# Kernel tuning notes

Measured on AMD Instinct MI355X. Metric: run time of the kernel, lower is better.

The kernel has to match this reference:

```python
import jax, jax.numpy as jnp
import numpy as np

B, S, M, H, P, T = 32, 400, 400, 200, 16, 4

def setup_inputs() -> dict:
    key = jax.random.key(0)
    ks = jax.random.split(key, 20)
    sc = 0.05
    inp = {
        'att': jax.random.normal(ks[0], (B, S, M), jnp.float32),
        'mod': jax.random.normal(ks[1], (B, S, M), jnp.float32),
        'mask': jnp.ones((B, S), jnp.float32),
        # LSTMCell: input 2*M, hidden H, gate order i,f,g,o
        'lstm_Wih': jax.random.normal(ks[2], (4 * H, 2 * M), jnp.float32) * sc,
        'lstm_Whh': jax.random.normal(ks[3], (4 * H, H), jnp.float32) * sc,
        'lstm_bih': jnp.zeros((4 * H,), jnp.float32),
        'lstm_bhh': jnp.zeros((4 * H,), jnp.float32),
    }
    for pfx, off in (('s', 4), ('e', 11)):
        inp[pfx + '_rW'] = jax.random.normal(ks[off + 0], (H, 2 * M + H), jnp.float32) * sc
        inp[pfx + '_W1'] = jax.random.normal(ks[off + 1], (P * H, M + H), jnp.float32) * sc
        inp[pfx + '_b1'] = jnp.zeros((P * H,), jnp.float32)
        inp[pfx + '_W2'] = jax.random.normal(ks[off + 2], (P * H, H), jnp.float32) * sc
        inp[pfx + '_b2'] = jnp.zeros((P * H,), jnp.float32)
        inp[pfx + '_W3'] = jax.random.normal(ks[off + 3], (P, 2 * H), jnp.float32) * sc
        inp[pfx + '_b3'] = jnp.zeros((P,), jnp.float32)
    return inp

def _gather(mod, idx):
    # mod:[B,S,M], idx:[B] -> [B,M]
    return jnp.take_along_axis(mod, idx[:, None, None], axis=1)[:, 0, :]

def _lstm_cell(x, h, c, Wih, Whh, bih, bhh):
    g = x @ Wih.T + bih + h @ Whh.T + bhh  # [B,4H]
    i, f, gg, o = jnp.split(g, 4, axis=1)
    c2 = jax.nn.sigmoid(f) * c + jax.nn.sigmoid(i) * jnp.tanh(gg)
    h2 = jax.nn.sigmoid(o) * jnp.tanh(c2)
    return h2, c2

def _hmn(mod, h, us, ue, mask, rW, W1, b1, W2, b2, W3, b3):
    r = jnp.tanh(jnp.concatenate([h, us, ue], 1) @ rW.T)  # [B,H]
    x = jnp.concatenate([mod, jnp.broadcast_to(r[:, None, :], (B, S, H))], 2)  # [B,S,M+H]
    m1 = (x @ W1.T + b1).reshape(B, S, P, H).max(2)   # maxout 1
    m2 = (m1 @ W2.T + b2).reshape(B, S, P, H).max(2)  # maxout 2
    logits = (jnp.concatenate([m1, m2], 2) @ W3.T + b3).max(2)  # [B,S]
    logits = jnp.where(mask > 0, logits, -1e30)
    return jax.nn.log_softmax(logits, axis=1)

def reference(att, mod, mask, lstm_Wih, lstm_Whh, lstm_bih, lstm_bhh,
              s_rW, s_W1, s_b1, s_W2, s_b2, s_W3, s_b3,
              e_rW, e_W1, e_b1, e_W2, e_b2, e_W3, e_b3):
    s_prev = jnp.zeros((B,), jnp.int32)
    e_prev = jnp.sum(mask, 1).astype(jnp.int32) - 1
    h = jnp.zeros((B, H), mod.dtype)
    c = jnp.zeros((B, H), mod.dtype)
    log_p1s, log_p2s = [], []
    for _ in range(T):
        u_s = _gather(mod, s_prev)
        u_e = _gather(mod, e_prev)
        h, c = _lstm_cell(jnp.concatenate([u_s, u_e], 1), h, c,
                          lstm_Wih, lstm_Whh, lstm_bih, lstm_bhh)
        lp1 = _hmn(mod, h, u_s, u_e, mask, s_rW, s_W1, s_b1, s_W2, s_b2, s_W3, s_b3)
        s_prev = jnp.argmax(lp1, axis=1).astype(jnp.int32)
        u_s = _gather(mod, s_prev)
        lp2 = _hmn(mod, h, u_s, u_e, mask, e_rW, e_W1, e_b1, e_W2, e_b2, e_W3, e_b3)
        e_prev = jnp.argmax(lp2, axis=1).astype(jnp.int32)
        log_p1s.append(lp1)
        log_p2s.append(lp2)
    return jnp.stack(log_p1s, 1), jnp.stack(log_p2s, 1)  # each [B,T,S]
```

## Files before the change

kernel.cpp:

```cpp
#include <hip/hip_runtime.h>
#include <math.h>

#define NB 32
#define NS 400
#define NM 400
#define NH 200
#define NP 16
#define NT 4
#define NBS (NB*NS)
#define NPH (NP*NH)
#define NPH2 3328
#define NJT 13
#define NX  (2*NM)
#define NG  (4*NH)
#define NR  (2*NM+NH)
#define K1  1280
#define K2  640

typedef __attribute__((ext_vector_type(8))) short short8v;
typedef __attribute__((ext_vector_type(4))) float f32x4;
typedef __attribute__((ext_vector_type(4))) unsigned short us4;
typedef unsigned short ushort;

__device__ __forceinline__ float sigf(float x){ return 1.0f/(1.0f+expf(-x)); }

__device__ __forceinline__ ushort f2bf(float x){
  union{float f; unsigned u;} v; v.f=x;
  unsigned r = v.u + 0x7fffu + ((v.u>>16)&1u);
  return (ushort)(r>>16);
}
__device__ __forceinline__ float bf2f(ushort u){
  union{float f; unsigned v;} x; x.v = ((unsigned)u)<<16; return x.f;
}
__device__ __forceinline__ float wave_sum(float v){
  #pragma unroll
  for (int o=32;o>0;o>>=1) v += __shfl_xor(v, o);
  return v;
}

__global__ __launch_bounds__(256) void init_kernel(const float* __restrict__ mask,
    float* __restrict__ h, float* __restrict__ c,
    int* __restrict__ sprev, int* __restrict__ eprev){
  int b = blockIdx.x, tid = threadIdx.x;
  __shared__ float red[256];
  float s = 0.f;
  for (int i=tid;i<NS;i+=256) s += mask[(size_t)b*NS+i];
  red[tid]=s; __syncthreads();
  for (int st=128;st>0;st>>=1){ if(tid<st) red[tid]+=red[tid+st]; __syncthreads(); }
  if (tid==0){ sprev[b]=0; eprev[b]=(int)red[0]-1; }
  for (int i=tid;i<NH;i+=256){ h[(size_t)b*NH+i]=0.f; c[(size_t)b*NH+i]=0.f; }
}

__global__ __launch_bounds__(256) void conv_mod_k(const float* __restrict__ in, ushort* __restrict__ out){
  for (size_t i = (size_t)blockIdx.x*256+threadIdx.x; i < (size_t)NBS*K1; i += (size_t)gridDim.x*256){
    int r = (int)(i/K1), k = (int)(i%K1);
    ushort v = 0;
    if (k < 3*NM){
      float x = in[(size_t)r*NM + (k % NM)];
      ushort h = f2bf(x);
      v = (k < NM || k >= 2*NM) ? h : f2bf(x - bf2f(h));
    }
    out[i] = v;
  }
}
__global__ __launch_bounds__(256) void conv_w1_k(const float* __restrict__ in, ushort* __restrict__ out){
  for (size_t i = (size_t)blockIdx.x*256+threadIdx.x; i < (size_t)NPH2*K1; i += (size_t)gridDim.x*256){
    int jp = (int)(i/K1), k = (int)(i%K1);
    ushort v = 0;
    if (jp < NPH && k < 3*NM){
      int j = (jp&15)*NH + (jp>>4);
      float x = in[(size_t)j*(NM+NH) + (k % NM)];
      ushort h = f2bf(x);
      v = (k < 2*NM) ? h : f2bf(x - bf2f(h));
    }
    out[i] = v;
  }
}
__global__ __launch_bounds__(256) void conv_w2_k(const float* __restrict__ in, ushort* __restrict__ out){
  for (size_t i = (size_t)blockIdx.x*256+threadIdx.x; i < (size_t)NPH2*K2; i += (size_t)gridDim.x*256){
    int jp = (int)(i/K2), k = (int)(i%K2);
    ushort v = 0;
    if (jp < NPH && k < 3*NH){
      int j = (jp&15)*NH + (jp>>4);
      float x = in[(size_t)j*NH + (k % NH)];
      ushort h = f2bf(x);
      v = (k < 2*NH) ? h : f2bf(x - bf2f(h));
    }
    out[i] = v;
  }
}
__global__ __launch_bounds__(256) void conv_w1r_k(const float* __restrict__ in, float* __restrict__ out){
  for (size_t i = (size_t)blockIdx.x*256+threadIdx.x; i < (size_t)NH*NPH; i += (size_t)gridDim.x*256){
    int k = (int)(i/NPH), jp = (int)(i%NPH);
    int hh = jp>>4, p = jp&15, j = p*NH + hh;
    out[i] = in[(size_t)j*(NM+NH) + NM + k];
  }
}
__global__ __launch_bounds__(256) void permv_k(const float* __restrict__ in, float* __restrict__ out){
  int i = blockIdx.x*256+threadIdx.x;
  if (i < NPH) out[(i%NH)*NP + i/NH] = in[i];
  else if (i < NPH2) out[i] = 0.f;
}
__global__ __launch_bounds__(256) void pad_zero_k(ushort* __restrict__ p, int stride, int start, int width, int rows){
  for (size_t i = (size_t)blockIdx.x*256+threadIdx.x; i < (size_t)rows*width; i += (size_t)gridDim.x*256){
    int r = (int)(i/width), j = (int)(i%width);
    p[(size_t)r*stride + start + j] = 0;
  }
}

__global__ __launch_bounds__(256) void lstm_gates(const float* __restrict__ mod,
    const int* __restrict__ sprev, const int* __restrict__ eprev,
    const float* __restrict__ h,
    const float* __restrict__ Wih, const float* __restrict__ Whh,
    const float* __restrict__ bih, const float* __restrict__ bhh,
    float* __restrict__ gs){
  int b=blockIdx.x, tid=threadIdx.x;
  __shared__ float xs[NX+NH];
  const float* us = mod + ((size_t)b*NS + sprev[b])*NM;
  const float* ue = mod + ((size_t)b*NS + eprev[b])*NM;
  for (int i=tid;i<NM;i+=256){ xs[i]=us[i]; xs[NM+i]=ue[i]; }
  for (int i=tid;i<NH;i+=256) xs[NX+i]=h[(size_t)b*NH+i];
  __syncthreads();
  int w=tid>>6, lane=tid&63;
  int j = blockIdx.y*4 + w;
  const float* wih = Wih + (size_t)j*NX;
  const float* whh = Whh + (size_t)j*NH;
  float acc=0.f;
  for (int k=lane;k<NX;k+=64) acc += xs[k]*wih[k];
  for (int k=lane;k<NH;k+=64) acc += xs[NX+k]*whh[k];
  acc = wave_sum(acc);
  if (lane==0) gs[(size_t)b*NG+j] = acc + bih[j] + bhh[j];
}
__global__ __launch_bounds__(256) void lstm_update(const float* __restrict__ gs,
    float* __restrict__ h, float* __restrict__ c){
  int b=blockIdx.x, j=threadIdx.x;
  if (j<NH){
    float iv=gs[(size_t)b*NG+j], fv=gs[(size_t)b*NG+NH+j];
    float gv=gs[(size_t)b*NG+2*NH+j], ov=gs[(size_t)b*NG+3*NH+j];
    float c2 = sigf(fv)*c[(size_t)b*NH+j] + sigf(iv)*tanhf(gv);
    c[(size_t)b*NH+j]=c2;
    h[(size_t)b*NH+j]=sigf(ov)*tanhf(c2);
  }
}

__global__ __launch_bounds__(256) void r_kernel(const float* __restrict__ mod,
    const int* __restrict__ sprev, const int* __restrict__ eprev,
    const float* __restrict__ h, const float* __restrict__ rW,
    float* __restrict__ rbuf){
  int b=blockIdx.x, tid=threadIdx.x;
  __shared__ float zs[NR];
  const float* us = mod + ((size_t)b*NS + sprev[b])*NM;
  const float* ue = mod + ((size_t)b*NS + eprev[b])*NM;
  for (int i=tid;i<NH;i+=256) zs[i]=h[(size_t)b*NH+i];
  for (int i=tid;i<NM;i+=256){ zs[NH+i]=us[i]; zs[NH+NM+i]=ue[i]; }
  __syncthreads();
  int w=tid>>6, lane=tid&63;
  int j = blockIdx.y*4 + w;
  const float* wr = rW + (size_t)j*NR;
  float acc=0.f;
  for (int k=lane;k<NR;k+=64) acc += zs[k]*wr[k];
  acc = wave_sum(acc);
  if (lane==0) rbuf[(size_t)b*NH+j] = tanhf(acc);
}

__global__ __launch_bounds__(256) void prer_kernel(const float* __restrict__ rbuf,
    const float* __restrict__ W1rT, const float* __restrict__ b1p,
    float* __restrict__ prer){
  int b=blockIdx.x, tid=threadIdx.x;
  __shared__ float rs[NH];
  if (tid < NH) rs[tid] = rbuf[(size_t)b*NH+tid];
  __syncthreads();
  int jp = blockIdx.y*256 + tid;
  if (jp < NPH2){
    float acc = 0.f;
    if (jp < NPH){
      acc = b1p[jp];
      #pragma unroll 8
      for (int k=0;k<NH;k++) acc += rs[k]*W1rT[(size_t)k*NPH + jp];
    }
    prer[(size_t)b*NPH2 + jp] = acc;
  }
}

template<int MODE>
__global__ __launch_bounds__(512, 2) void gemm_fused(
    const ushort* __restrict__ A, const ushort* __restrict__ W,
    const float* __restrict__ bias, void* __restrict__ outp){
  constexpr int LDK = (MODE==1) ? K2 : K1;
  constexpr int NTI = LDK/32;
  __shared__ __align__(16) ushort As[4][256*32];
  __shared__ __align__(16) ushort Bs[4][256*32];
  __shared__ float biasLds[2][256];
  __shared__ float outT[256][16];
  const int tid = threadIdx.x;
  const int nwg = gridDim.x;
  const int q = nwg >> 3, r = nwg & 7;
  const int xcd = blockIdx.x & 7, sub = blockIdx.x >> 3;
  const int wkid = (xcd < r) ? (xcd*(q+1) + sub) : (r*(q+1) + (xcd-r)*q + sub);
  const int i0 = (wkid / NJT) * 256, j0 = (wkid % NJT) * 256;
  const int b0 = i0/NS;
  if (MODE==0){
    if (tid<256) biasLds[0][tid] = bias[(size_t)b0*NPH2 + j0 + tid];
    else { int b1r=(i0+255)/NS; biasLds[1][tid-256] = bias[(size_t)b1r*NPH2 + j0 + (tid-256)]; }
  } else if (MODE==1){
    if (tid<256) biasLds[0][tid] = bias[j0+tid];
  }
  const int w = tid>>6, l = tid&63;
  const int wr = w>>2, wc = w&3;
  const int fr = l&15, fk = l>>4;
  const int srow = w*32 + (l>>2);
  const int sslot = l&3;
  const int swzc = (sslot ^ ((srow>>1)&3))*8;
  const ushort* gA0 = A + (size_t)(i0+srow)*LDK + swzc;
  const ushort* gB0 = W + (size_t)(j0+srow)*LDK + swzc;
  const int ldsOff = srow*32 + sslot*8;
  auto stage = [&](int slot, int kt){
    const ushort* a = gA0 + kt*32;
    const ushort* b = gB0 + kt*32;
    __builtin_amdgcn_global_load_lds((const __attribute__((address_space(1))) void*)a,
        (__attribute__((address_space(3))) void*)(&As[slot][ldsOff]), 16, 0, 0);
    __builtin_amdgcn_global_load_lds((const __attribute__((address_space(1))) void*)(a + 16*LDK),
        (__attribute__((address_space(3))) void*)(&As[slot][ldsOff + 16*32]), 16, 0, 0);
    __builtin_amdgcn_global_load_lds((const __attribute__((address_space(1))) void*)b,
        (__attribute__((address_space(3))) void*)(&Bs[slot][ldsOff]), 16, 0, 0);
    __builtin_amdgcn_global_load_lds((const __attribute__((address_space(1))) void*)(b + 16*LDK),
        (__attribute__((address_space(3))) void*)(&Bs[slot][ldsOff + 16*32]), 16, 0, 0);
  };
  f32x4 acc[8][4] = {};
  stage(0,0); stage(1,1); stage(2,2);
  for (int t=0; t<NTI; t++){
    if (t+2 < NTI)      asm volatile("s_waitcnt vmcnt(8)\n\ts_barrier" ::: "memory");
    else if (t+1 < NTI) asm volatile("s_waitcnt vmcnt(4)\n\ts_barrier" ::: "memory");
    else                asm volatile("s_waitcnt vmcnt(0)\n\ts_barrier" ::: "memory");
    const int s = t&3;
    short8v a[8], b[4];
    #pragma unroll
    for (int m=0;m<8;m++){
      int row = wr*128 + m*16 + fr;
      a[m] = *(const short8v*)&As[s][row*32 + ((fk ^ ((row>>1)&3))*8)];
    }
    #pragma unroll
    for (int n=0;n<4;n++){
      int row = wc*64 + n*16 + fr;
      b[n] = *(const short8v*)&Bs[s][row*32 + ((fk ^ ((row>>1)&3))*8)];
    }
    if (t+3 < NTI) stage((t+3)&3, t+3);
    __builtin_amdgcn_s_setprio(1);
    #pragma unroll
    for (int m=0;m<8;m++)
      #pragma unroll
      for (int n=0;n<4;n++)
        acc[m][n] = __builtin_amdgcn_mfma_f32_16x16x32_bf16(a[m], b[n], acc[m][n], 0,0,0);
    __builtin_amdgcn_s_setprio(0);
  }
  if (MODE==2){
    float* o = (float*)outp;
    #pragma unroll
    for (int m=0;m<8;m++){
      #pragma unroll
      for (int n=0;n<4;n++){
        int col = j0 + wc*64 + n*16 + fr;
        if (col < NPH){
          int rbase = i0 + wr*128 + m*16 + fk*4;
          #pragma unroll
          for (int reg=0;reg<4;reg++)
            o[(size_t)(rbase+reg)*NPH + col] = acc[m][n][reg];
        }
      }
    }
    return;
  }
  __syncthreads();
  const int blim = (b0+1)*NS;
  #pragma unroll
  for (int m=0;m<8;m++){
    #pragma unroll
    for (int n=0;n<4;n++){
      int colL = wc*64 + n*16 + fr;
      int rbase = wr*128 + m*16 + fk*4;
      #pragma unroll
      for (int reg=0; reg<4; reg++){
        int rowL = rbase + reg;
        float bv = (MODE==0 && (i0+rowL) >= blim) ? biasLds[1][colL] : biasLds[0][colL];
        float v = acc[m][n][reg] + bv;
        v = fmaxf(v, __shfl_xor(v,1));
        v = fmaxf(v, __shfl_xor(v,2));
        v = fmaxf(v, __shfl_xor(v,4));
        v = fmaxf(v, __shfl_xor(v,8));
        if (fr==0) outT[rowL][wc*4+n] = v;
      }
    }
  }
  __syncthreads();
  {
    int rowL = tid>>1;
    int hloc0 = (tid&1)*8;
    int hg0 = (j0>>4) + hloc0;
    if (hg0 < NH){
      int absrow = i0 + rowL;
      float v[8];
      #pragma unroll
      for (int qq=0;qq<8;qq++) v[qq] = outT[rowL][hloc0+qq];
      if (MODE==0){
        ushort* o = (ushort*)outp + (size_t)absrow*K2 + hg0;
        ushort hi[8], lo[8];
        #pragma unroll
        for (int qq=0;qq<8;qq++){ hi[qq]=f2bf(v[qq]); lo[qq]=f2bf(v[qq]-bf2f(hi[qq])); }
        *(us4*)(o)        = (us4){hi[0],hi[1],hi[2],hi[3]};
        *(us4*)(o+4)      = (us4){hi[4],hi[5],hi[6],hi[7]};
        *(us4*)(o+NH)     = (us4){lo[0],lo[1],lo[2],lo[3]};
        *(us4*)(o+NH+4)   = (us4){lo[4],lo[5],lo[6],lo[7]};
        *(us4*)(o+2*NH)   = (us4){hi[0],hi[1],hi[2],hi[3]};
        *(us4*)(o+2*NH+4) = (us4){hi[4],hi[5],hi[6],hi[7]};
      } else {
        float* o = (float*)outp + (size_t)absrow*NH + hg0;
        *(f32x4*)o     = (f32x4){v[0],v[1],v[2],v[3]};
        *(f32x4*)(o+4) = (f32x4){v[4],v[5],v[6],v[7]};
      }
    }
  }
}

__global__ __launch_bounds__(256) void maxp_kernel(const float* __restrict__ premod,
    const float* __restrict__ prer, ushort* __restrict__ m1e){
  int i = blockIdx.x;
  int b = i / NS;
  int h = threadIdx.x;
  if (h >= NH) return;
  const float* pm = premod + (size_t)i*NPH + h*16;
  const float* pr = prer + (size_t)b*NPH2 + h*16;
  float v = -INFINITY;
  #pragma unroll
  for (int p=0;p<16;p+=4){
    f32x4 a = *(const f32x4*)(pm+p);
    f32x4 c = *(const f32x4*)(pr+p);
    v = fmaxf(v, fmaxf(fmaxf(a.x+c.x, a.y+c.y), fmaxf(a.z+c.z, a.w+c.w)));
  }
  ushort hi = f2bf(v), lo = f2bf(v - bf2f(hi));
  ushort* o = m1e + (size_t)i*K2;
  o[h] = hi; o[NH+h] = lo; o[2*NH+h] = hi;
}

__global__ __launch_bounds__(256) void logits_main(const ushort* __restrict__ m1e,
    const float* __restrict__ m2, const float* __restrict__ W3, const float* __restrict__ b3,
    const float* __restrict__ mask, float* __restrict__ lg){
  int b=blockIdx.x;
  int s=blockIdx.y*256+threadIdx.x;
  if (s >= NS) return;
  const ushort* a = m1e + (size_t)(b*NS+s)*K2;
  const float4* d = (const float4*)(m2 + (size_t)(b*NS+s)*NH);
  float acc[NP];
  #pragma unroll
  for (int p=0;p<NP;p++) acc[p]=b3[p];
  for (int k=0;k<NH/4;k++){
    us4 hv = *(const us4*)(a + 4*k);
    us4 lv = *(const us4*)(a + NH + 4*k);
    float4 dv = d[k];
    float a0=bf2f(hv.x)+bf2f(lv.x), a1=bf2f(hv.y)+bf2f(lv.y);
    float a2=bf2f(hv.z)+bf2f(lv.z), a3=bf2f(hv.w)+bf2f(lv.w);
    #pragma unroll
    for (int p=0;p<NP;p++){
      const float* wp = W3 + p*(2*NH) + 4*k;
      acc[p] += a0*wp[0]+a1*wp[1]+a2*wp[2]+a3*wp[3];
      const float* w2 = wp + NH;
      acc[p] += dv.x*w2[0]+dv.y*w2[1]+dv.z*w2[2]+dv.w*w2[3];
    }
  }
  float best=acc[0];
  #pragma unroll
  for (int p=1;p<NP;p++) best=fmaxf(best,acc[p]);
  lg[(size_t)b*NS+s] = (mask[(size_t)b*NS+s] > 0.f) ? best : -1e30f;
}

__global__ __launch_bounds__(256) void logits_fin(const float* __restrict__ lg,
    float* __restrict__ out, int t, int* __restrict__ prevIdx){
  int b=blockIdx.x, tid=threadIdx.x;
  __shared__ float rv[256]; __shared__ int ri[256]; __shared__ float sv[256];
  float bv=-INFINITY; int bi=NS;
  for (int s=tid;s<NS;s+=256){ float v=lg[(size_t)b*NS+s]; if (v>bv){bv=v;bi=s;} }
  rv[tid]=bv; ri[tid]=bi; __syncthreads();
  for (int st=128;st>0;st>>=1){
    if (tid<st){
      float v2=rv[tid+st]; int i2=ri[tid+st];
      if (v2>rv[tid] || (v2==rv[tid] && i2<ri[tid])){ rv[tid]=v2; ri[tid]=i2; }
    }
    __syncthreads();
  }
  float mx = rv[0];
  float ps=0.f;
  for (int s=tid;s<NS;s+=256) ps += expf(lg[(size_t)b*NS+s]-mx);
  sv[tid]=ps; __syncthreads();
  for (int st=128;st>0;st>>=1){ if (tid<st) sv[tid]+=sv[tid+st]; __syncthreads(); }
  float lse = mx + logf(sv[0]);
  for (int s=tid;s<NS;s+=256) out[((size_t)b*NT + t)*NS + s] = lg[(size_t)b*NS+s]-lse;
  if (tid==0) prevIdx[b]=ri[0];
}

extern "C" void kernel_launch(void* const* d_in, const int* in_sizes, int n_in,
                              void* d_out, int out_size, void* d_ws, size_t ws_size,
                              hipStream_t stream){
  const float* mod  = (const float*)d_in[1];
  const float* mask = (const float*)d_in[2];
  const float* Wih  = (const float*)d_in[3];
  const float* Whh  = (const float*)d_in[4];
  const float* bih  = (const float*)d_in[5];
  const float* bhh  = (const float*)d_in[6];
  const float* rW[2] = {(const float*)d_in[7],  (const float*)d_in[14]};
  const float* W1[2] = {(const float*)d_in[8],  (const float*)d_in[15]};
  const float* b1[2] = {(const float*)d_in[9],  (const float*)d_in[16]};
  const float* W2[2] = {(const float*)d_in[10], (const float*)d_in[17]};
  const float* b2[2] = {(const float*)d_in[11], (const float*)d_in[18]};
  const float* W3[2] = {(const float*)d_in[12], (const float*)d_in[19]};
  const float* b3[2] = {(const float*)d_in[13], (const float*)d_in[20]};
  float* out[2];
  out[0] = (float*)d_out;
  out[1] = out[0] + (size_t)NB*NT*NS;

  float* wsf = (float*)d_ws;
  size_t off = 0;
  auto carve = [&](size_t n)->size_t{ size_t o=off; off += (n + 63) & ~(size_t)63; return o; };
  float* hbuf   = wsf + carve((size_t)NB*NH);
  float* cbuf   = wsf + carve((size_t)NB*NH);
  float* prer   = wsf + carve((size_t)NB*NPH2);
  int*   sprev  = (int*)(wsf + carve(128));
  int*   eprev  = sprev + 32;
  float* m2f    = wsf + carve((size_t)NBS*NH);
  float* b2p[2] = {wsf + carve(NPH2), wsf + carve(NPH2)};
  float* b1p[2] = {wsf + carve(NPH2), wsf + carve(NPH2)};
  float* rbuf   = wsf + carve((size_t)NB*NH);
  float* gsbuf  = wsf + carve((size_t)NB*NG);
  float* lgbuf  = wsf + carve((size_t)NB*NS);
  float* W1rT[2]= {wsf + carve((size_t)NH*NPH), wsf + carve((size_t)NH*NPH)};
  ushort* modExp   = (ushort*)(wsf + carve((size_t)NBS*K1/2));
  ushort* W1exp[2] = {(ushort*)(wsf + carve((size_t)NPH2*K1/2)),
                      (ushort*)(wsf + carve((size_t)NPH2*K1/2))};
  ushort* W2exp[2] = {(ushort*)(wsf + carve((size_t)NPH2*K2/2)),
                      (ushort*)(wsf + carve((size_t)NPH2*K2/2))};
  ushort* m1exp    = (ushort*)(wsf + carve((size_t)NBS*K2/2));

  const size_t premodN = (size_t)NBS * NPH;
  size_t availF = ws_size / 4;
  int nHoist = 0;
  float* premod[2] = {nullptr, nullptr};
  if (availF >= off + 2*premodN + 128){
    nHoist = 2; premod[0] = wsf + carve(premodN); premod[1] = wsf + carve(premodN);
  } else if (availF >= off + premodN + 128){
    nHoist = 1; premod[0] = wsf + carve(premodN);
  }

  init_kernel<<<NB, 256, 0, stream>>>(mask, hbuf, cbuf, sprev, eprev);
  conv_mod_k<<<2048, 256, 0, stream>>>(mod, modExp);
  pad_zero_k<<<256, 256, 0, stream>>>(m1exp, K2, 3*NH, K2-3*NH, NBS);
  for (int net=0; net<2; net++){
    conv_w1_k<<<2048, 256, 0, stream>>>(W1[net], W1exp[net]);
    conv_w2_k<<<1024, 256, 0, stream>>>(W2[net], W2exp[net]);
    conv_w1r_k<<<1024, 256, 0, stream>>>(W1[net], W1rT[net]);
    permv_k<<<(NPH2+255)/256, 256, 0, stream>>>(b2[net], b2p[net]);
    permv_k<<<(NPH2+255)/256, 256, 0, stream>>>(b1[net], b1p[net]);
  }
  for (int net=0; net<nHoist; net++)
    gemm_fused<2><<<NBS/256*NJT, 512, 0, stream>>>(modExp, W1exp[net], nullptr, (void*)premod[net]);

  for (int t=0; t<NT; t++){
    lstm_gates<<<dim3(NB, NG/4), 256, 0, stream>>>(mod, sprev, eprev, hbuf,
                                                   Wih, Whh, bih, bhh, gsbuf);
    lstm_update<<<NB, 256, 0, stream>>>(gsbuf, hbuf, cbuf);
    for (int net=0; net<2; net++){
      r_kernel<<<dim3(NB, NH/4), 256, 0, stream>>>(mod, sprev, eprev, hbuf, rW[net], rbuf);
      prer_kernel<<<dim3(NB, NPH2/256), 256, 0, stream>>>(rbuf, W1rT[net], b1p[net], prer);
      if (net < nHoist)
        maxp_kernel<<<NBS, 256, 0, stream>>>(premod[net], prer, m1exp);
      else
        gemm_fused<0><<<NBS/256*NJT, 512, 0, stream>>>(modExp, W1exp[net], prer, (void*)m1exp);
      gemm_fused<1><<<NBS/256*NJT, 512, 0, stream>>>(m1exp, W2exp[net], b2p[net], (void*)m2f);
      logits_main<<<dim3(NB, 2), 256, 0, stream>>>(m1exp, m2f, W3[net], b3[net], mask, lgbuf);
      logits_fin<<<NB, 256, 0, stream>>>(lgbuf, out[net], t, net==0 ? sprev : eprev);
    }
  }
}
```

Before: 2.671 ms.

## Restructure GEMM mainloop to double-buffered BK=64 tiles with LDS union

The bf16 MFMA GEMM mainloop changes from a 4-stage ring of 32-wide K tiles to a 2-stage double buffer of 64-wide K tiles, with an 8-way XOR swizzle and two MFMA sub-steps per barrier. Barriers per K step are halved, but the loop now waits for all outstanding loads before each step, so prefetch depth drops from three tiles to one. The epilogue's transpose buffer is unioned with the staging buffers to save LDS, and the launch bound's min-blocks hint is dropped, which may change register allocation and occupancy.

Result: slower. 3.639 ms (+36.2%).

```diff
diff --git a/kernel.cpp b/kernel.cpp
--- a/kernel.cpp
+++ b/kernel.cpp
@@ -183,15 +183,15 @@
 }
 
 template<int MODE>
-__global__ __launch_bounds__(512, 2) void gemm_fused(
+__global__ __launch_bounds__(512) void gemm_fused(
     const ushort* __restrict__ A, const ushort* __restrict__ W,
     const float* __restrict__ bias, void* __restrict__ outp){
   constexpr int LDK = (MODE==1) ? K2 : K1;
-  constexpr int NTI = LDK/32;
-  __shared__ __align__(16) ushort As[4][256*32];
-  __shared__ __align__(16) ushort Bs[4][256*32];
+  constexpr int NTI = LDK/64;
+  struct SMs { ushort A[2][256*64]; ushort B[2][256*64]; };
+  union SMu { SMs s; float outT[256][16]; };
+  __shared__ SMu sm;
   __shared__ float biasLds[2][256];
-  __shared__ float outT[256][16];
   const int tid = threadIdx.x;
   const int nwg = gridDim.x;
   const int q = nwg >> 3, r = nwg & 7;
@@ -208,50 +208,50 @@
   const int w = tid>>6, l = tid&63;
   const int wr = w>>2, wc = w&3;
   const int fr = l&15, fk = l>>4;
-  const int srow = w*32 + (l>>2);
-  const int sslot = l&3;
-  const int swzc = (sslot ^ ((srow>>1)&3))*8;
-  const ushort* gA0 = A + (size_t)(i0+srow)*LDK + swzc;
-  const ushort* gB0 = W + (size_t)(j0+srow)*LDK + swzc;
-  const int ldsOff = srow*32 + sslot*8;
+  const int srow = tid>>3, ss = tid&7;
+  const int swzc = (ss ^ (srow&7))*8;
+  const ushort* gA = A + (size_t)(i0+srow)*LDK + swzc;
+  const ushort* gB = W + (size_t)(j0+srow)*LDK + swzc;
+  const int ldsD = tid*8;
   auto stage = [&](int slot, int kt){
-    const ushort* a = gA0 + kt*32;
-    const ushort* b = gB0 + kt*32;
-    __builtin_amdgcn_global_load_lds((const __attribute__((address_space(1))) void*)a,
-        (__attribute__((address_space(3))) void*)(&As[slot][ldsOff]), 16, 0, 0);
-    __builtin_amdgcn_global_load_lds((const __attribute__((address_space(1))) void*)(a + 16*LDK),
-        (__attribute__((address_space(3))) void*)(&As[slot][ldsOff + 16*32]), 16, 0, 0);
-    __builtin_amdgcn_global_load_lds((const __attribute__((address_space(1))) void*)b,
-        (__attribute__((address_space(3))) void*)(&Bs[slot][ldsOff]), 16, 0, 0);
-    __builtin_amdgcn_global_load_lds((const __attribute__((address_space(1))) void*)(b + 16*LDK),
-        (__attribute__((address_space(3))) void*)(&Bs[slot][ldsOff + 16*32]), 16, 0, 0);
+    const ushort* a = gA + kt*64;
+    #pragma unroll
+    for (int j=0;j<4;j++)
+      __builtin_amdgcn_global_load_lds((const __attribute__((address_space(1))) void*)(a + (size_t)(j*64)*LDK),
+          (__attribute__((address_space(3))) void*)(&sm.s.A[slot][j*4096 + ldsD]), 16, 0, 0);
+    const ushort* b = gB + kt*64;
+    #pragma unroll
+    for (int j=0;j<4;j++)
+      __builtin_amdgcn_global_load_lds((const __attribute__((address_space(1))) void*)(b + (size_t)(j*64)*LDK),
+          (__attribute__((address_space(3))) void*)(&sm.s.B[slot][j*4096 + ldsD]), 16, 0, 0);
   };
   f32x4 acc[8][4] = {};
-  stage(0,0); stage(1,1); stage(2,2);
+  stage(0,0);
   for (int t=0; t<NTI; t++){
-    if (t+2 < NTI)      asm volatile("s_waitcnt vmcnt(8)\n\ts_barrier" ::: "memory");
-    else if (t+1 < NTI) asm volatile("s_waitcnt vmcnt(4)\n\ts_barrier" ::: "memory");
-    else                asm volatile("s_waitcnt vmcnt(0)\n\ts_barrier" ::: "memory");
-    const int s = t&3;
-    short8v a[8], b[4];
-    #pragma unroll
-    for (int m=0;m<8;m++){
-      int row = wr*128 + m*16 + fr;
-      a[m] = *(const short8v*)&As[s][row*32 + ((fk ^ ((row>>1)&3))*8)];
-    }
-    #pragma unroll
-    for (int n=0;n<4;n++){
-      int row = wc*64 + n*16 + fr;
-      b[n] = *(const short8v*)&Bs[s][row*32 + ((fk ^ ((row>>1)&3))*8)];
-    }
-    if (t+3 < NTI) stage((t+3)&3, t+3);
-    __builtin_amdgcn_s_setprio(1);
-    #pragma unroll
-    for (int m=0;m<8;m++)
-      #pragma unroll
-      for (int n=0;n<4;n++)
-        acc[m][n] = __builtin_amdgcn_mfma_f32_16x16x32_bf16(a[m], b[n], acc[m][n], 0,0,0);
-    __builtin_amdgcn_s_setprio(0);
+    const int s = t&1;
+    asm volatile("s_waitcnt vmcnt(0)\n\ts_barrier" ::: "memory");
+    if (t+1 < NTI) stage(s^1, t+1);
+    #pragma unroll
+    for (int ks=0; ks<2; ks++){
+      short8v a8[8], b8[4];
+      #pragma unroll
+      for (int m=0;m<8;m++){
+        int row = wr*128 + m*16 + fr;
+        a8[m] = *(const short8v*)&sm.s.A[s][row*64 + (((ks*4+fk) ^ (row&7))<<3)];
+      }
+      #pragma unroll
+      for (int n=0;n<4;n++){
+        int row = wc*64 + n*16 + fr;
+        b8[n] = *(const short8v*)&sm.s.B[s][row*64 + (((ks*4+fk) ^ (row&7))<<3)];
+      }
+      __builtin_amdgcn_s_setprio(1);
+      #pragma unroll
+      for (int m=0;m<8;m++)
+        #pragma unroll
+        for (int n=0;n<4;n++)
+          acc[m][n] = __builtin_amdgcn_mfma_f32_16x16x32_bf16(a8[m], b8[n], acc[m][n], 0,0,0);
+      __builtin_amdgcn_s_setprio(0);
+    }
   }
   if (MODE==2){
     float* o = (float*)outp;
@@ -287,7 +287,7 @@
         v = fmaxf(v, __shfl_xor(v,2));
         v = fmaxf(v, __shfl_xor(v,4));
         v = fmaxf(v, __shfl_xor(v,8));
-        if (fr==0) outT[rowL][wc*4+n] = v;
+        if (fr==0) sm.outT[rowL][wc*4+n] = v;
       }
     }
   }
@@ -300,7 +300,7 @@
       int absrow = i0 + rowL;
       float v[8];
       #pragma unroll
-      for (int qq=0;qq<8;qq++) v[qq] = outT[rowL][hloc0+qq];
+      for (int qq=0;qq<8;qq++) v[qq] = sm.outT[rowL][hloc0+qq];
       if (MODE==0){
         ushort* o = (ushort*)outp + (size_t)absrow*K2 + hg0;
         ushort hi[8], lo[8];
@@ -458,8 +458,9 @@
     permv_k<<<(NPH2+255)/256, 256, 0, stream>>>(b2[net], b2p[net]);
     permv_k<<<(NPH2+255)/256, 256, 0, stream>>>(b1[net], b1p[net]);
   }
+  const int GGRID = (NBS/256) * NJT;
   for (int net=0; net<nHoist; net++)
-    gemm_fused<2><<<NBS/256*NJT, 512, 0, stream>>>(modExp, W1exp[net], nullptr, (void*)premod[net]);
+    gemm_fused<2><<<GGRID, 512, 0, stream>>>(modExp, W1exp[net], nullptr, (void*)premod[net]);
 
   for (int t=0; t<NT; t++){
     lstm_gates<<<dim3(NB, NG/4), 256, 0, stream>>>(mod, sprev, eprev, hbuf,
@@ -471,8 +472,8 @@
       if (net < nHoist)
         maxp_kernel<<<NBS, 256, 0, stream>>>(premod[net], prer, m1exp);
       else
-        gemm_fused<0><<<NBS/256*NJT, 512, 0, stream>>>(modExp, W1exp[net], prer, (void*)m1exp);
-      gemm_fused<1><<<NBS/256*NJT, 512, 0, stream>>>(m1exp, W2exp[net], b2p[net], (void*)m2f);
+        gemm_fused<0><<<GGRID, 512, 0, stream>>>(modExp, W1exp[net], prer, (void*)m1exp);
+      gemm_fused<1><<<GGRID, 512, 0, stream>>>(m1exp, W2exp[net], b2p[net], (void*)m2f);
       logits_main<<<dim3(NB, 2), 256, 0, stream>>>(m1exp, m2f, W3[net], b3[net], mask, lgbuf);
       logits_fin<<<NB, 256, 0, stream>>>(lgbuf, out[net], t, net==0 ? sprev : eprev);
     }
```

## Drop hoisted W1 precompute path and shrink padded GEMM K dimensions

Applied to the files above, without the earlier changes.

Removes the path that precomputed mod@W1 once per net into a large fp32 buffer and applied a per-step max kernel, so the fused W1 GEMM with maxout now runs every step. It also shrinks the padded K extents of the split-bf16 GEMM operands (K1 and K2) and lowers the conversion-kernel grid sizes to match. The K reduction cuts MFMA and load work per GEMM. Dropping the hoist avoids the big premod write and reread, but redoes the full W1 GEMM at every step.

Result: slower. 2.968 ms (+11.1%).

```diff
diff --git a/kernel.cpp b/kernel.cpp
--- a/kernel.cpp
+++ b/kernel.cpp
@@ -14,8 +14,8 @@
 #define NX  (2*NM)
 #define NG  (4*NH)
 #define NR  (2*NM+NH)
-#define K1  1280
-#define K2  640
+#define K1  1216
+#define K2  608
 
 typedef __attribute__((ext_vector_type(8))) short short8v;
 typedef __attribute__((ext_vector_type(4))) float f32x4;
@@ -202,7 +202,7 @@
   if (MODE==0){
     if (tid<256) biasLds[0][tid] = bias[(size_t)b0*NPH2 + j0 + tid];
     else { int b1r=(i0+255)/NS; biasLds[1][tid-256] = bias[(size_t)b1r*NPH2 + j0 + (tid-256)]; }
-  } else if (MODE==1){
+  } else {
     if (tid<256) biasLds[0][tid] = bias[j0+tid];
   }
   const int w = tid>>6, l = tid&63;
@@ -253,23 +253,6 @@
         acc[m][n] = __builtin_amdgcn_mfma_f32_16x16x32_bf16(a[m], b[n], acc[m][n], 0,0,0);
     __builtin_amdgcn_s_setprio(0);
   }
-  if (MODE==2){
-    float* o = (float*)outp;
-    #pragma unroll
-    for (int m=0;m<8;m++){
-      #pragma unroll
-      for (int n=0;n<4;n++){
-        int col = j0 + wc*64 + n*16 + fr;
-        if (col < NPH){
-          int rbase = i0 + wr*128 + m*16 + fk*4;
-          #pragma unroll
-          for (int reg=0;reg<4;reg++)
-            o[(size_t)(rbase+reg)*NPH + col] = acc[m][n][reg];
-        }
-      }
-    }
-    return;
-  }
   __syncthreads();
   const int blim = (b0+1)*NS;
   #pragma unroll
@@ -321,26 +304,6 @@
   }
 }
 
-__global__ __launch_bounds__(256) void maxp_kernel(const float* __restrict__ premod,
-    const float* __restrict__ prer, ushort* __restrict__ m1e){
-  int i = blockIdx.x;
-  int b = i / NS;
-  int h = threadIdx.x;
-  if (h >= NH) return;
-  const float* pm = premod + (size_t)i*NPH + h*16;
-  const float* pr = prer + (size_t)b*NPH2 + h*16;
-  float v = -INFINITY;
-  #pragma unroll
-  for (int p=0;p<16;p+=4){
-    f32x4 a = *(const f32x4*)(pm+p);
-    f32x4 c = *(const f32x4*)(pr+p);
-    v = fmaxf(v, fmaxf(fmaxf(a.x+c.x, a.y+c.y), fmaxf(a.z+c.z, a.w+c.w)));
-  }
-  ushort hi = f2bf(v), lo = f2bf(v - bf2f(hi));
-  ushort* o = m1e + (size_t)i*K2;
-  o[h] = hi; o[NH+h] = lo; o[2*NH+h] = hi;
-}
-
 __global__ __launch_bounds__(256) void logits_main(const ushort* __restrict__ m1e,
     const float* __restrict__ m2, const float* __restrict__ W3, const float* __restrict__ b3,
     const float* __restrict__ mask, float* __restrict__ lg){
@@ -438,29 +401,18 @@
                       (ushort*)(wsf + carve((size_t)NPH2*K2/2))};
   ushort* m1exp    = (ushort*)(wsf + carve((size_t)NBS*K2/2));
 
-  const size_t premodN = (size_t)NBS * NPH;
-  size_t availF = ws_size / 4;
-  int nHoist = 0;
-  float* premod[2] = {nullptr, nullptr};
-  if (availF >= off + 2*premodN + 128){
-    nHoist = 2; premod[0] = wsf + carve(premodN); premod[1] = wsf + carve(premodN);
-  } else if (availF >= off + premodN + 128){
-    nHoist = 1; premod[0] = wsf + carve(premodN);
-  }
-
   init_kernel<<<NB, 256, 0, stream>>>(mask, hbuf, cbuf, sprev, eprev);
   conv_mod_k<<<2048, 256, 0, stream>>>(mod, modExp);
-  pad_zero_k<<<256, 256, 0, stream>>>(m1exp, K2, 3*NH, K2-3*NH, NBS);
+  pad_zero_k<<<128, 256, 0, stream>>>(m1exp, K2, 3*NH, K2-3*NH, NBS);
   for (int net=0; net<2; net++){
-    conv_w1_k<<<2048, 256, 0, stream>>>(W1[net], W1exp[net]);
-    conv_w2_k<<<1024, 256, 0, stream>>>(W2[net], W2exp[net]);
+    conv_w1_k<<<1024, 256, 0, stream>>>(W1[net], W1exp[net]);
+    conv_w2_k<<<512, 256, 0, stream>>>(W2[net], W2exp[net]);
     conv_w1r_k<<<1024, 256, 0, stream>>>(W1[net], W1rT[net]);
     permv_k<<<(NPH2+255)/256, 256, 0, stream>>>(b2[net], b2p[net]);
     permv_k<<<(NPH2+255)/256, 256, 0, stream>>>(b1[net], b1p[net]);
   }
-  for (int net=0; net<nHoist; net++)
-    gemm_fused<2><<<NBS/256*NJT, 512, 0, stream>>>(modExp, W1exp[net], nullptr, (void*)premod[net]);
-
+
+  const int GFULL = (NBS/256) * NJT;
   for (int t=0; t<NT; t++){
     lstm_gates<<<dim3(NB, NG/4), 256, 0, stream>>>(mod, sprev, eprev, hbuf,
                                                    Wih, Whh, bih, bhh, gsbuf);
@@ -468,11 +420,8 @@
     for (int net=0; net<2; net++){
       r_kernel<<<dim3(NB, NH/4), 256, 0, stream>>>(mod, sprev, eprev, hbuf, rW[net], rbuf);
       prer_kernel<<<dim3(NB, NPH2/256), 256, 0, stream>>>(rbuf, W1rT[net], b1p[net], prer);
-      if (net < nHoist)
-        maxp_kernel<<<NBS, 256, 0, stream>>>(premod[net], prer, m1exp);
-      else
-        gemm_fused<0><<<NBS/256*NJT, 512, 0, stream>>>(modExp, W1exp[net], prer, (void*)m1exp);
-      gemm_fused<1><<<NBS/256*NJT, 512, 0, stream>>>(m1exp, W2exp[net], b2p[net], (void*)m2f);
+      gemm_fused<0><<<GFULL, 512, 0, stream>>>(modExp, W1exp[net], prer, (void*)m1exp);
+      gemm_fused<1><<<GFULL, 512, 0, stream>>>(m1exp, W2exp[net], b2p[net], (void*)m2f);
       logits_main<<<dim3(NB, 2), 256, 0, stream>>>(m1exp, m2f, W3[net], b3[net], mask, lgbuf);
       logits_fin<<<NB, 256, 0, stream>>>(lgbuf, out[net], t, net==0 ? sprev : eprev);
     }
```
